# Kernel optimization log

Measured on AMD Instinct MI355X. Metric: run time of the kernel, lower is better.

Reference implementation:

```python
import jax, jax.numpy as jnp
import numpy as np

N_NODES = 50000
N_EDGES = 600000
HID = 128
OUT = 14
LAYERS = 3
N_GRAPHS = 16
NODE_VOCAB = (120, 6)
EDGE_VOCAB = (6, 3)
GEN_EPS = 1e-7   # GENConv eps added after ReLU on messages
BN_EPS = 1e-5    # torch BatchNorm1d default eps


def setup_inputs() -> dict:
    key = jax.random.key(0)
    ks = jax.random.split(key, 14)
    inp = {}
    inp['node_feat0'] = jax.random.randint(ks[0], (N_NODES,), 0, NODE_VOCAB[0], dtype=jnp.int32)
    inp['node_feat1'] = jax.random.randint(ks[1], (N_NODES,), 0, NODE_VOCAB[1], dtype=jnp.int32)
    inp['edge_feat0'] = jax.random.randint(ks[2], (N_EDGES,), 0, EDGE_VOCAB[0], dtype=jnp.int32)
    inp['edge_feat1'] = jax.random.randint(ks[3], (N_EDGES,), 0, EDGE_VOCAB[1], dtype=jnp.int32)
    inp['edge_src'] = jax.random.randint(ks[4], (N_EDGES,), 0, N_NODES, dtype=jnp.int32)
    inp['edge_dst'] = jax.random.randint(ks[5], (N_EDGES,), 0, N_NODES, dtype=jnp.int32)
    inp['graph_ids'] = jnp.repeat(jnp.arange(N_GRAPHS, dtype=jnp.int32), N_NODES // N_GRAPHS)
    inp['num_graphs'] = N_GRAPHS
    s = 0.05
    inp['W_node0'] = jax.random.normal(ks[6], (NODE_VOCAB[0], HID), jnp.float32) * s
    inp['W_node1'] = jax.random.normal(ks[7], (NODE_VOCAB[1], HID), jnp.float32) * s
    # per-layer edge embedding tables (each GENConv layer has its own)
    inp['edge_emb0'] = jax.random.normal(ks[8], (LAYERS, EDGE_VOCAB[0], HID), jnp.float32) * s
    inp['edge_emb1'] = jax.random.normal(ks[9], (LAYERS, EDGE_VOCAB[1], HID), jnp.float32) * s
    inp['beta'] = jnp.ones((LAYERS,), jnp.float32)  # learnable softmax temperature, init 1.0
    inp['mlp_W'] = jax.random.normal(ks[10], (LAYERS, HID, HID), jnp.float32) * (1.0 / np.sqrt(HID))
    inp['mlp_b'] = jnp.zeros((LAYERS, HID), jnp.float32)
    inp['bn_gamma'] = jnp.ones((LAYERS, HID), jnp.float32)
    inp['bn_beta'] = jnp.zeros((LAYERS, HID), jnp.float32)
    inp['W_out'] = jax.random.normal(ks[11], (HID, OUT), jnp.float32) * (1.0 / np.sqrt(HID))
    inp['b_out'] = jnp.zeros((OUT,), jnp.float32)
    return inp


def _segment_softmax(z, seg, num_segments):
    # DGL edge_softmax: elementwise softmax over edges sharing a destination node.
    zmax = jax.ops.segment_max(z, seg, num_segments=num_segments)
    zmax = jnp.where(jnp.isfinite(zmax), zmax, 0.0)  # guard empty segments
    e = jnp.exp(z - zmax[seg])
    denom = jax.ops.segment_sum(e, seg, num_segments=num_segments)
    return e / denom[seg]


def reference(node_feat0, node_feat1, edge_feat0, edge_feat1, edge_src, edge_dst,
              graph_ids, num_graphs, W_node0, W_node1, edge_emb0, edge_emb1,
              beta, mlp_W, mlp_b, bn_gamma, bn_beta, W_out, b_out):
    # node embedding lookup + sum over tables
    hv = W_node0[node_feat0] + W_node1[node_feat1]          # [N, H]
    n = hv.shape[0]
    for l in range(mlp_W.shape[0]):
        # BatchNorm1d (training mode: batch stats, biased variance) + ReLU
        mu = jnp.mean(hv, axis=0)
        var = jnp.var(hv, axis=0)
        hv1 = (hv - mu) * jax.lax.rsqrt(var + BN_EPS) * bn_gamma[l] + bn_beta[l]
        hv1 = jax.nn.relu(hv1)
        # GENConv: edge embed sum, u_add_e, relu+eps, edge_softmax, scatter-sum
        ee = edge_emb0[l][edge_feat0] + edge_emb1[l][edge_feat1]   # [E, H]
        m = jax.nn.relu(hv1[edge_src] + ee) + GEN_EPS              # [E, H]
        a = _segment_softmax(m * beta[l], edge_dst, n)             # [E, H]
        agg = jax.ops.segment_sum(m * a, edge_dst, num_segments=n)  # [N, H]
        # feats = node_feats + msg, then 1-layer MLP, then outer skip connect
        hv = (hv1 + agg) @ mlp_W[l] + mlp_b[l] + hv
    # AvgPooling over each graph in the batch, then output Linear
    counts = jax.ops.segment_sum(jnp.ones((n,), hv.dtype), graph_ids, num_segments=num_graphs)
    hg = jax.ops.segment_sum(hv, graph_ids, num_segments=num_graphs) / counts[:, None]
    return hg @ W_out + b_out  # [num_graphs, OUT]
```

## Files before the change

kernel.cpp:

```cpp
#include <hip/hip_runtime.h>

#define N_NODESC 50000
#define N_EDGESC 600000
#define HID 128
#define LAYERS 3
#define N_GRAPHSC 16
#define OUT_DIM 14
#define GEN_EPS 1e-7f
#define BN_EPS 1e-5f
#define SCAN_BLK 196
#define EMB_BLK 6250
#define WF_BLK 192
#define CNT_BLK 2344
#define GEMM_BLK 782
#define BNR_BLK 512
#define EDGE_CAP 1792
#define LOG2E 1.44269504f

typedef short bf16x8 __attribute__((ext_vector_type(8)));
typedef float f32x4 __attribute__((ext_vector_type(4)));

__device__ __forceinline__ unsigned short f2bf(float f) {
    union { float f; unsigned u; } v; v.f = f;
    unsigned r = v.u + 0x7FFF + ((v.u >> 16) & 1);
    return (unsigned short)(r >> 16);
}
__device__ __forceinline__ float bf_lo(unsigned u) {
    return __uint_as_float(u << 16);
}
__device__ __forceinline__ float bf_hi(unsigned u) {
    return __uint_as_float(u & 0xFFFF0000u);
}
__device__ __forceinline__ float bfs(unsigned short u) {
    return __uint_as_float(((unsigned)u) << 16);
}

__global__ void k_csrbn(const int* __restrict__ deg, const float* __restrict__ part,
                        int* __restrict__ row_ptr, int* __restrict__ cursor,
                        int* __restrict__ gctr, float* __restrict__ gsum) {
    int t = threadIdx.x;
    if (blockIdx.x >= SCAN_BLK) {
        int b = blockIdx.x - SCAN_BLK;
        const int rows = (EMB_BLK + BNR_BLK - 1) / BNR_BLK;
        int r0 = b * rows;
        int r1 = min(r0 + rows, EMB_BLK);
        float s = 0.f;
        for (int p = r0; p < r1; p++) s += part[(size_t)p * 256 + t];
        atomicAdd(&gsum[t], s);
        return;
    }
    __shared__ int sh[256];
    __shared__ int sbase;
    int i = blockIdx.x * 256 + t;
    int d = (i < N_NODESC) ? deg[i] : 0;
    sh[t] = d;
    __syncthreads();
    for (int off = 1; off < 256; off <<= 1) {
        int add = (t >= off) ? sh[t - off] : 0;
        __syncthreads();
        sh[t] += add;
        __syncthreads();
    }
    if (t == 255) sbase = atomicAdd(gctr, sh[255]);
    __syncthreads();
    if (i < N_NODESC) {
        int rp = sbase + sh[t] - d;
        row_ptr[i] = rp;
        cursor[i] = rp;
    }
}

__global__ void k_scatter(const int* __restrict__ dst, const int* __restrict__ src,
                          const int* __restrict__ f0, const int* __restrict__ f1,
                          int* __restrict__ cursor, int* __restrict__ csr_pack) {
    int i = blockIdx.x * blockDim.x + threadIdx.x;
    if (i < N_EDGESC) {
        int pos = atomicAdd(&cursor[dst[i]], 1);
        csr_pack[pos] = (src[i] << 8) | ((f0[i] * 3 + f1[i]) * 8);
    }
}

__global__ void k_embed(const int* __restrict__ f0, const int* __restrict__ f1,
                        const float4* __restrict__ W0, const float4* __restrict__ W1,
                        uint2* __restrict__ hvb2, float* __restrict__ part,
                        const float* __restrict__ W, unsigned short* __restrict__ wf,
                        const int* __restrict__ edst, int* __restrict__ deg) {
    int tid = threadIdx.x;
    if (blockIdx.x >= EMB_BLK + WF_BLK) {
        int e = (blockIdx.x - EMB_BLK - WF_BLK) * 256 + tid;
        if (e < N_EDGESC) atomicAdd(&deg[edst[e]], 1);
        return;
    }
    if (blockIdx.x >= EMB_BLK) {
        int i = (blockIdx.x - EMB_BLK) * 256 + tid;
        if (i < LAYERS * 16384) {
            int j = i & 7;
            int lane = (i >> 3) & 63;
            int nt = (i >> 9) & 7;
            int ks = (i >> 12) & 3;
            int l = i >> 14;
            int k = ks * 32 + (lane >> 4) * 8 + j;
            int n = nt * 16 + (lane & 15);
            wf[i] = f2bf(W[(size_t)l * HID * HID + k * HID + n]);
        }
        return;
    }
    __shared__ float sh[1024], sh2[1024];
    int i = blockIdx.x * 256 + tid;
    int v = i >> 5, c4 = i & 31;
    float4 a = W0[f0[v] * 32 + c4];
    float4 b = W1[f1[v] * 32 + c4];
    float4 o = make_float4(a.x + b.x, a.y + b.y, a.z + b.z, a.w + b.w);
    uint2 ob;
    ob.x = (unsigned)f2bf(o.x) | ((unsigned)f2bf(o.y) << 16);
    ob.y = (unsigned)f2bf(o.z) | ((unsigned)f2bf(o.w) << 16);
    hvb2[i] = ob;
    sh[tid * 4 + 0] = o.x; sh2[tid * 4 + 0] = o.x * o.x;
    sh[tid * 4 + 1] = o.y; sh2[tid * 4 + 1] = o.y * o.y;
    sh[tid * 4 + 2] = o.z; sh2[tid * 4 + 2] = o.z * o.z;
    sh[tid * 4 + 3] = o.w; sh2[tid * 4 + 3] = o.w * o.w;
    __syncthreads();
    if (tid < 128) {
        int c4i = tid >> 2, j = tid & 3;
        float s = 0.f, s2 = 0.f;
#pragma unroll
        for (int r = 0; r < 8; r++) {
            s += sh[(r * 32 + c4i) * 4 + j];
            s2 += sh2[(r * 32 + c4i) * 4 + j];
        }
        part[(size_t)blockIdx.x * 256 + tid] = s;
        part[(size_t)blockIdx.x * 256 + 128 + tid] = s2;
    }
}

__global__ __launch_bounds__(1024) void k_aggemm(
    const unsigned* __restrict__ hin, unsigned short* __restrict__ hout,
    const int* __restrict__ row_ptr, const int* __restrict__ degp,
    const int* __restrict__ csr_pack,
    const float* __restrict__ e0, const float* __restrict__ e1,
    const float* __restrict__ beta_p, const unsigned short* __restrict__ wf,
    const float* __restrict__ b, const float* __restrict__ gsum,
    const float* __restrict__ gamma, const float* __restrict__ betab,
    float* __restrict__ gsum_next, float* __restrict__ hg) {
    __shared__ float2 sh_et[18 * 64];
    __shared__ unsigned x_tile[64 * 64];
    __shared__ float shs[512], shs2[512];
    __shared__ int sh_pack[EDGE_CAP + 8];
    __shared__ int sh_rp[64];
    __shared__ int sh_deg[64];
    __shared__ int row_ctr;
    int tid = threadIdx.x;
    for (int i = tid; i < 18 * 64; i += 1024) {
        int f = i >> 6, ln = i & 63;
        int a = f / 3, bb = f - 3 * a;
        float2 ea = *(const float2*)(e0 + a * HID + 2 * ln);
        float2 eb = *(const float2*)(e1 + bb * HID + 2 * ln);
        sh_et[i] = make_float2(ea.x + eb.x, ea.y + eb.y);
    }
    int w = tid >> 6, lane = tid & 63;
    int m0 = blockIdx.x * 64;
    if (tid < 64) {
        int v = m0 + tid;
        sh_rp[tid] = row_ptr[min(v, N_NODESC - 1)];
        sh_deg[tid] = (v < N_NODESC) ? degp[v] : 0;
    }
    if (tid == 0) row_ctr = 0;
    int eb0 = row_ptr[m0];
    int rl = min(m0 + 63, N_NODESC - 1);
    int nE = min(row_ptr[rl] + degp[rl] - eb0, EDGE_CAP);
    for (int i = tid; i < nE; i += 1024) sh_pack[i] = csr_pack[eb0 + i];
    if (tid < 8) sh_pack[nE + tid] = 0;

    const float bl2 = (*beta_p) * LOG2E;
    const float invN = 1.f / (float)N_NODESC;
    int cch = lane * 2;
    float mu0 = gsum[cch] * invN, mu1 = gsum[cch + 1] * invN;
    float var0 = gsum[128 + cch] * invN - mu0 * mu0;
    float var1 = gsum[129 + cch] * invN - mu1 * mu1;
    float sc0 = gamma[cch] * rsqrtf(var0 + BN_EPS);
    float sc1 = gamma[cch + 1] * rsqrtf(var1 + BN_EPS);
    float sf0 = betab[cch] - mu0 * sc0;
    float sf1 = betab[cch + 1] - mu1 * sc1;
    __syncthreads();

    const char* hinc = (const char*)hin;
    const char* etc = (const char*)sh_et;
    unsigned lane4 = (unsigned)lane * 4;
    unsigned lane8 = (unsigned)lane * 8;

#define GATH(S, PK)                                                         \
    unsigned u##S = *(const unsigned*)(hinc +                               \
                        ((((unsigned)(PK)) & 0xFFFFFF00u) + lane4));        \
    float2 t##S = *(const float2*)(etc +                                    \
                        (((((unsigned)(PK)) & 0xFFu) << 6) + lane8));
#define CMP(S, VAL)                                                         \
    {                                                                       \
        float a0 = fmaxf(fmaf(bf_lo(u##S), sc0, sf0), 0.f);                 \
        float a1 = fmaxf(fmaf(bf_hi(u##S), sc1, sf1), 0.f);                 \
        float r0 = fmaxf(a0 + t##S.x, 0.f);                                 \
        float r1 = fmaxf(a1 + t##S.y, 0.f);                                 \
        float ei0 = (VAL) ? (r0 * bl2) : -1000.f;                           \
        float ei1 = (VAL) ? (r1 * bl2) : -1000.f;                           \
        float w0 = exp2f(ei0);                                              \
        float w1 = exp2f(ei1);                                              \
        d0 += w0; d1 += w1;                                                 \
        n0 = fmaf(r0, w0, n0); n1 = fmaf(r1, w1, n1);                       \
    }

    for (;;) {
        int rsel = 0;
        if (lane == 0) rsel = atomicAdd(&row_ctr, 1);
        rsel = __builtin_amdgcn_readfirstlane(rsel);
        if (rsel >= 64) break;
        int row = rsel;
        int v = m0 + row;
        int vc = min(v, N_NODESC - 1);
        unsigned su = hin[(size_t)vc * 64 + lane];
        float h10 = fmaxf(fmaf(bf_lo(su), sc0, sf0), 0.f);
        float h11 = fmaxf(fmaf(bf_hi(su), sc1, sf1), 0.f);
        int p0 = sh_rp[row] - eb0;
        int deg = sh_deg[row];
        float n0 = 0.f, n1 = 0.f, d0 = 0.f, d1 = 0.f;
        if (p0 + deg <= nE) {
            for (int j0 = 0; j0 < deg; j0 += 4) {
                int i0 = p0 + j0;
                int pkA = sh_pack[i0];
                int pkB = sh_pack[i0 + 1];
                int pkC = sh_pack[i0 + 2];
                int pkD = sh_pack[i0 + 3];
                GATH(A, pkA) GATH(B, pkB) GATH(C, pkC) GATH(D, pkD)
                int rem = deg - j0;
                CMP(A, true)
                CMP(B, rem > 1)
                CMP(C, rem > 2)
                CMP(D, rem > 3)
            }
        } else {
            int last = p0 + deg - 1;
            for (int j0 = 0; j0 < deg; j0 += 4) {
                int i0 = p0 + j0;
                int pkA = csr_pack[eb0 + i0];
                int pkB = csr_pack[eb0 + min(i0 + 1, last)];
                int pkC = csr_pack[eb0 + min(i0 + 2, last)];
                int pkD = csr_pack[eb0 + min(i0 + 3, last)];
                GATH(A, pkA) GATH(B, pkB) GATH(C, pkC) GATH(D, pkD)
                int rem = deg - j0;
                CMP(A, true)
                CMP(B, rem > 1)
                CMP(C, rem > 2)
                CMP(D, rem > 3)
            }
        }
        float ox = h10 + (deg ? __fdividef(n0, d0) + GEN_EPS : 0.f);
        float oy = h11 + (deg ? __fdividef(n1, d1) + GEN_EPS : 0.f);
        x_tile[row * 64 + ((lane + row * 4) & 63)] =
            (unsigned)f2bf(ox) | ((unsigned)f2bf(oy) << 16);
    }
#undef GATH
#undef CMP
    __syncthreads();

    int rw = w & 3, chh = w >> 2;
    int mrow = lane & 15, grp = lane >> 4;
    int rbase = rw * 16 + mrow;
    bf16x8 af[4];
#pragma unroll
    for (int ks = 0; ks < 4; ks++) {
        int col = ks * 16 + grp * 4;
        int colr = (col + rbase * 4) & 63;
        af[ks] = *(const bf16x8*)&x_tile[rbase * 64 + colr];
    }
    f32x4 acc[2];
#pragma unroll
    for (int nt = 0; nt < 2; nt++) acc[nt] = (f32x4){0.f, 0.f, 0.f, 0.f};
#pragma unroll
    for (int nt = 0; nt < 2; nt++) {
        int ntg = chh * 2 + nt;
#pragma unroll
        for (int ks = 0; ks < 4; ks++) {
            bf16x8 bfr = *(const bf16x8*)(wf +
                (size_t)((ks * 8 + ntg) * 64 + lane) * 8);
            acc[nt] = __builtin_amdgcn_mfma_f32_16x16x32_bf16(
                af[ks], bfr, acc[nt], 0, 0, 0);
        }
    }
    const unsigned short* hin_s = (const unsigned short*)hin;
    int gA = m0 / 3125;
    int boundary = (gA + 1) * 3125;
#pragma unroll
    for (int nt = 0; nt < 2; nt++) {
        int col = chh * 32 + nt * 16 + mrow;
        float bias = b[col];
        float s = 0.f, s2 = 0.f;
#pragma unroll
        for (int r = 0; r < 4; r++) {
            int v = m0 + rw * 16 + grp * 4 + r;
            if (v < N_NODESC) {
                size_t idx = (size_t)v * HID + col;
                float o = acc[nt][r] + bias + bfs(hin_s[idx]);
                hout[idx] = f2bf(o);
                if (hg) {
                    if (v < boundary) s += o; else s2 += o;
                } else {
                    s += o; s2 += o * o;
                }
            }
        }
        s  += __shfl_xor(s, 16, 64);  s  += __shfl_xor(s, 32, 64);
        s2 += __shfl_xor(s2, 16, 64); s2 += __shfl_xor(s2, 32, 64);
        if (lane < 16) { shs[rw * 128 + col] = s; shs2[rw * 128 + col] = s2; }
    }
    __syncthreads();
    if (hg) {
        int gB = min(m0 + 63, N_NODESC - 1) / 3125;
        if (tid < 128) {
            atomicAdd(&hg[gA * 128 + tid],
                shs[tid] + shs[128 + tid] + shs[256 + tid] + shs[384 + tid]);
        } else if (tid < 256 && gB != gA) {
            int c = tid - 128;
            atomicAdd(&hg[gB * 128 + c],
                shs2[c] + shs2[128 + c] + shs2[256 + c] + shs2[384 + c]);
        }
    } else if (gsum_next) {
        if (tid < 128) {
            atomicAdd(&gsum_next[tid],
                shs[tid] + shs[128 + tid] + shs[256 + tid] + shs[384 + tid]);
        } else if (tid < 256) {
            int c = tid - 128;
            atomicAdd(&gsum_next[tid],
                shs2[c] + shs2[128 + c] + shs2[256 + c] + shs2[384 + c]);
        }
    }
}

__global__ void k_finish(const float* __restrict__ hg, const float* __restrict__ Wo,
                         const float* __restrict__ bo, float* __restrict__ out) {
    int t = threadIdx.x;
    if (t >= N_GRAPHSC * OUT_DIM) return;
    int g = t / OUT_DIM, o = t % OUT_DIM;
    const float inv = (float)N_GRAPHSC / (float)N_NODESC;
    float acc = bo[o];
    for (int k = 0; k < HID; k++)
        acc += hg[g * HID + k] * inv * Wo[k * OUT_DIM + o];
    out[t] = acc;
}

extern "C" void kernel_launch(void* const* d_in, const int* in_sizes, int n_in,
                              void* d_out, int out_size, void* d_ws, size_t ws_size,
                              hipStream_t stream) {
    const int* node_feat0 = (const int*)d_in[0];
    const int* node_feat1 = (const int*)d_in[1];
    const int* edge_feat0 = (const int*)d_in[2];
    const int* edge_feat1 = (const int*)d_in[3];
    const int* edge_src   = (const int*)d_in[4];
    const int* edge_dst   = (const int*)d_in[5];
    const float* W_node0   = (const float*)d_in[8];
    const float* W_node1   = (const float*)d_in[9];
    const float* edge_emb0 = (const float*)d_in[10];
    const float* edge_emb1 = (const float*)d_in[11];
    const float* beta      = (const float*)d_in[12];
    const float* mlp_W     = (const float*)d_in[13];
    const float* mlp_b     = (const float*)d_in[14];
    const float* bn_gamma  = (const float*)d_in[15];
    const float* bn_beta   = (const float*)d_in[16];
    const float* W_out     = (const float*)d_in[17];
    const float* b_out     = (const float*)d_in[18];
    float* out = (float*)d_out;

    char* ws = (char*)d_ws;
    size_t off = 0;
    auto alloc = [&](size_t bytes) -> void* {
        void* p = ws + off;
        off += (bytes + 255) & ~(size_t)255;
        return p;
    };
    unsigned short* hvA = (unsigned short*)alloc((size_t)N_NODESC * HID * 2);
    unsigned short* hvB = (unsigned short*)alloc((size_t)N_NODESC * HID * 2);
    float* gsums   = (float*)alloc(LAYERS * 256 * 4);
    float* hg      = (float*)alloc(N_GRAPHSC * HID * 4);
    int*   gctr    = (int*)alloc(256);
    float* bnpart  = (float*)alloc((size_t)EMB_BLK * 256 * 4);
    unsigned short* wfrag = (unsigned short*)alloc((size_t)LAYERS * 16384 * 2);
    int* row_ptr   = (int*)alloc((N_NODESC + 1) * 4);
    int* cursor    = (int*)alloc(N_NODESC * 4);
    int* deg       = (int*)alloc(N_NODESC * 4);
    int* csr_pack  = (int*)alloc((size_t)N_EDGESC * 4 + 64);

    hipMemsetAsync(deg, 0, N_NODESC * 4, stream);
    hipMemsetAsync(gsums, 0, LAYERS * 256 * 4 + N_GRAPHSC * HID * 4 + 256, stream);

    k_embed<<<EMB_BLK + WF_BLK + CNT_BLK, 256, 0, stream>>>(
        node_feat0, node_feat1, (const float4*)W_node0, (const float4*)W_node1,
        (uint2*)hvA, bnpart, mlp_W, wfrag, edge_dst, deg);

    k_csrbn<<<SCAN_BLK + BNR_BLK, 256, 0, stream>>>(
        deg, bnpart, row_ptr, cursor, gctr, gsums);

    k_scatter<<<(N_EDGESC + 255) / 256, 256, 0, stream>>>(
        edge_dst, edge_src, edge_feat0, edge_feat1, cursor, csr_pack);

    unsigned short* hin = hvA;
    unsigned short* hout = hvB;
    for (int l = 0; l < LAYERS; l++) {
        float* gsum = gsums + l * 256;
        float* gnext = (l + 1 < LAYERS) ? gsums + (l + 1) * 256 : nullptr;
        float* hgp = (l == LAYERS - 1) ? hg : nullptr;
        k_aggemm<<<GEMM_BLK, 1024, 0, stream>>>(
            (const unsigned*)hin, hout, row_ptr, deg, csr_pack,
            edge_emb0 + (size_t)l * 6 * HID, edge_emb1 + (size_t)l * 3 * HID,
            beta + l, wfrag + (size_t)l * 16384, mlp_b + l * HID,
            gsum, bn_gamma + l * HID, bn_beta + l * HID, gnext, hgp);
        unsigned short* tmp = hin; hin = hout; hout = tmp;
    }

    k_finish<<<1, 256, 0, stream>>>(hg, W_out, b_out, out);
}
```

Measured before the change: 374.9 us.

## Fuse final linear into last layer, merge memsets, vectorize scatter, split accumulators

Drops the separate k_finish launch: the last block of the final aggregation layer, found with an atomic done-counter, computes the output linear. The two memsets become one by placing deg next to the other zeroed buffers. The scatter kernel handles two edges per thread with int2 loads. The softmax accumulators are split into four independent chains to shorten FMA dependency chains, which adds register pressure.

```diff
diff --git a/kernel.cpp b/kernel.cpp
--- a/kernel.cpp
+++ b/kernel.cpp
@@ -73,8 +73,17 @@
 __global__ void k_scatter(const int* __restrict__ dst, const int* __restrict__ src,
                           const int* __restrict__ f0, const int* __restrict__ f1,
                           int* __restrict__ cursor, int* __restrict__ csr_pack) {
-    int i = blockIdx.x * blockDim.x + threadIdx.x;
-    if (i < N_EDGESC) {
+    int i = (blockIdx.x * blockDim.x + threadIdx.x) * 2;
+    if (i + 1 < N_EDGESC) {
+        int2 d2 = *(const int2*)(dst + i);
+        int2 s2 = *(const int2*)(src + i);
+        int2 a2 = *(const int2*)(f0 + i);
+        int2 b2 = *(const int2*)(f1 + i);
+        int p0 = atomicAdd(&cursor[d2.x], 1);
+        csr_pack[p0] = (s2.x << 8) | ((a2.x * 3 + b2.x) * 8);
+        int p1 = atomicAdd(&cursor[d2.y], 1);
+        csr_pack[p1] = (s2.y << 8) | ((a2.y * 3 + b2.y) * 8);
+    } else if (i < N_EDGESC) {
         int pos = atomicAdd(&cursor[dst[i]], 1);
         csr_pack[pos] = (src[i] << 8) | ((f0[i] * 3 + f1[i]) * 8);
     }
@@ -141,7 +150,9 @@
     const float* __restrict__ beta_p, const unsigned short* __restrict__ wf,
     const float* __restrict__ b, const float* __restrict__ gsum,
     const float* __restrict__ gamma, const float* __restrict__ betab,
-    float* __restrict__ gsum_next, float* __restrict__ hg) {
+    float* __restrict__ gsum_next, float* __restrict__ hg,
+    const float* __restrict__ Wo, const float* __restrict__ bo,
+    float* __restrict__ outp, int* __restrict__ done) {
     __shared__ float2 sh_et[18 * 64];
     __shared__ unsigned x_tile[64 * 64];
     __shared__ float shs[512], shs2[512];
@@ -149,6 +160,7 @@
     __shared__ int sh_rp[64];
     __shared__ int sh_deg[64];
     __shared__ int row_ctr;
+    __shared__ int lastf;
     int tid = threadIdx.x;
     for (int i = tid; i < 18 * 64; i += 1024) {
         int f = i >> 6, ln = i & 63;
@@ -203,8 +215,9 @@
         float ei1 = (VAL) ? (r1 * bl2) : -1000.f;                           \
         float w0 = exp2f(ei0);                                              \
         float w1 = exp2f(ei1);                                              \
-        d0 += w0; d1 += w1;                                                 \
-        n0 = fmaf(r0, w0, n0); n1 = fmaf(r1, w1, n1);                       \
+        d##S##0 += w0; d##S##1 += w1;                                       \
+        n##S##0 = fmaf(r0, w0, n##S##0);                                    \
+        n##S##1 = fmaf(r1, w1, n##S##1);                                    \
     }
 
     for (;;) {
@@ -220,7 +233,10 @@
         float h11 = fmaxf(fmaf(bf_hi(su), sc1, sf1), 0.f);
         int p0 = sh_rp[row] - eb0;
         int deg = sh_deg[row];
-        float n0 = 0.f, n1 = 0.f, d0 = 0.f, d1 = 0.f;
+        float nA0 = 0.f, nA1 = 0.f, dA0 = 0.f, dA1 = 0.f;
+        float nB0 = 0.f, nB1 = 0.f, dB0 = 0.f, dB1 = 0.f;
+        float nC0 = 0.f, nC1 = 0.f, dC0 = 0.f, dC1 = 0.f;
+        float nD0 = 0.f, nD1 = 0.f, dD0 = 0.f, dD1 = 0.f;
         if (p0 + deg <= nE) {
             for (int j0 = 0; j0 < deg; j0 += 4) {
                 int i0 = p0 + j0;
@@ -251,6 +267,10 @@
                 CMP(D, rem > 3)
             }
         }
+        float n0 = (nA0 + nB0) + (nC0 + nD0);
+        float n1 = (nA1 + nB1) + (nC1 + nD1);
+        float d0 = (dA0 + dB0) + (dC0 + dD0);
+        float d1 = (dA1 + dB1) + (dC1 + dD1);
         float ox = h10 + (deg ? __fdividef(n0, d0) + GEN_EPS : 0.f);
         float oy = h11 + (deg ? __fdividef(n1, d1) + GEN_EPS : 0.f);
         x_tile[row * 64 + ((lane + row * 4) & 63)] =
@@ -321,6 +341,26 @@
             atomicAdd(&hg[gB * 128 + c],
                 shs2[c] + shs2[128 + c] + shs2[256 + c] + shs2[384 + c]);
         }
+        __threadfence();
+        if (tid == 0) {
+            int old = atomicAdd(done, 1);
+            lastf = (old == GEMM_BLK - 1) ? 1 : 0;
+        }
+        __syncthreads();
+        if (lastf) {
+            float* shg = (float*)x_tile;
+            for (int i = tid; i < N_GRAPHSC * HID; i += 1024)
+                shg[i] = atomicAdd(&hg[i], 0.0f);
+            __syncthreads();
+            if (tid < N_GRAPHSC * OUT_DIM) {
+                int g = tid / OUT_DIM, o = tid % OUT_DIM;
+                const float inv = (float)N_GRAPHSC / (float)N_NODESC;
+                float acc2 = bo[o];
+                for (int k = 0; k < HID; k++)
+                    acc2 += shg[g * HID + k] * inv * Wo[k * OUT_DIM + o];
+                outp[tid] = acc2;
+            }
+        }
     } else if (gsum_next) {
         if (tid < 128) {
             atomicAdd(&gsum_next[tid],
@@ -331,18 +371,6 @@
                 shs2[c] + shs2[128 + c] + shs2[256 + c] + shs2[384 + c]);
         }
     }
-}
-
-__global__ void k_finish(const float* __restrict__ hg, const float* __restrict__ Wo,
-                         const float* __restrict__ bo, float* __restrict__ out) {
-    int t = threadIdx.x;
-    if (t >= N_GRAPHSC * OUT_DIM) return;
-    int g = t / OUT_DIM, o = t % OUT_DIM;
-    const float inv = (float)N_GRAPHSC / (float)N_NODESC;
-    float acc = bo[o];
-    for (int k = 0; k < HID; k++)
-        acc += hg[g * HID + k] * inv * Wo[k * OUT_DIM + o];
-    out[t] = acc;
 }
 
 extern "C" void kernel_launch(void* const* d_in, const int* in_sizes, int n_in,
@@ -374,29 +402,29 @@
         off += (bytes + 255) & ~(size_t)255;
         return p;
     };
+    float* gsums   = (float*)alloc(LAYERS * 256 * 4);
+    float* hg      = (float*)alloc(N_GRAPHSC * HID * 4);
+    int*   ctrs    = (int*)alloc(256);
+    int*   deg     = (int*)alloc(N_NODESC * 4);
+    size_t zlen = LAYERS * 256 * 4 + N_GRAPHSC * HID * 4 + 256 + 200192;
+    float* bnpart  = (float*)alloc((size_t)EMB_BLK * 256 * 4);
     unsigned short* hvA = (unsigned short*)alloc((size_t)N_NODESC * HID * 2);
     unsigned short* hvB = (unsigned short*)alloc((size_t)N_NODESC * HID * 2);
-    float* gsums   = (float*)alloc(LAYERS * 256 * 4);
-    float* hg      = (float*)alloc(N_GRAPHSC * HID * 4);
-    int*   gctr    = (int*)alloc(256);
-    float* bnpart  = (float*)alloc((size_t)EMB_BLK * 256 * 4);
     unsigned short* wfrag = (unsigned short*)alloc((size_t)LAYERS * 16384 * 2);
     int* row_ptr   = (int*)alloc((N_NODESC + 1) * 4);
     int* cursor    = (int*)alloc(N_NODESC * 4);
-    int* deg       = (int*)alloc(N_NODESC * 4);
     int* csr_pack  = (int*)alloc((size_t)N_EDGESC * 4 + 64);
 
-    hipMemsetAsync(deg, 0, N_NODESC * 4, stream);
-    hipMemsetAsync(gsums, 0, LAYERS * 256 * 4 + N_GRAPHSC * HID * 4 + 256, stream);
+    hipMemsetAsync(gsums, 0, zlen, stream);
 
     k_embed<<<EMB_BLK + WF_BLK + CNT_BLK, 256, 0, stream>>>(
         node_feat0, node_feat1, (const float4*)W_node0, (const float4*)W_node1,
         (uint2*)hvA, bnpart, mlp_W, wfrag, edge_dst, deg);
 
     k_csrbn<<<SCAN_BLK + BNR_BLK, 256, 0, stream>>>(
-        deg, bnpart, row_ptr, cursor, gctr, gsums);
-
-    k_scatter<<<(N_EDGESC + 255) / 256, 256, 0, stream>>>(
+        deg, bnpart, row_ptr, cursor, ctrs, gsums);
+
+    k_scatter<<<(N_EDGESC / 2 + 255) / 256, 256, 0, stream>>>(
         edge_dst, edge_src, edge_feat0, edge_feat1, cursor, csr_pack);
 
     unsigned short* hin = hvA;
@@ -404,14 +432,15 @@
     for (int l = 0; l < LAYERS; l++) {
         float* gsum = gsums + l * 256;
         float* gnext = (l + 1 < LAYERS) ? gsums + (l + 1) * 256 : nullptr;
-        float* hgp = (l == LAYERS - 1) ? hg : nullptr;
+        int lastl = (l == LAYERS - 1);
         k_aggemm<<<GEMM_BLK, 1024, 0, stream>>>(
             (const unsigned*)hin, hout, row_ptr, deg, csr_pack,
             edge_emb0 + (size_t)l * 6 * HID, edge_emb1 + (size_t)l * 3 * HID,
             beta + l, wfrag + (size_t)l * 16384, mlp_b + l * HID,
-            gsum, bn_gamma + l * HID, bn_beta + l * HID, gnext, hgp);
+            gsum, bn_gamma + l * HID, bn_beta + l * HID, gnext,
+            lastl ? hg : nullptr,
+            lastl ? W_out : nullptr, lastl ? b_out : nullptr,
+            lastl ? out : nullptr, ctrs + 1);
         unsigned short* tmp = hin; hin = hout; hout = tmp;
     }
-
-    k_finish<<<1, 256, 0, stream>>>(hg, W_out, b_out, out);
-}
+}
```

New measurement: 643.3 us. 71.6% more time.
